# Kernel tuning notes

Measured on AMD Instinct MI355X. Metric: run time of the kernel, lower is better.

The kernel has to match this reference:

```python
import jax, jax.numpy as jnp
import numpy as np

EPS = 1e-8
BLOCK = 10  # proposals per frame; block-diagonal zeroing granularity


def _l2norm(x):
    # torch.norm(x, dim=-1, keepdim=True) + 1e-8
    return x / (jnp.linalg.norm(x, axis=-1, keepdims=True) + EPS)


def _block_mask(N):
    # For row j: zero cols [ (j//10)*10 , (j//10)*10 + 9 ) (i.e. 9 cols), then restore the diagonal.
    rows = jnp.arange(N)[:, None]
    cols = jnp.arange(N)[None, :]
    bstart = (rows // BLOCK) * BLOCK
    zeroed = (cols >= bstart) & (cols < bstart + (BLOCK - 1))
    keep = (~zeroed) | (rows == cols)
    return keep.astype(jnp.float32)  # [N, N]


def setup_inputs() -> dict:
    key = jax.random.key(0)
    k1, k2, k3, k4 = jax.random.split(key, 4)
    B, N, C = 1, 2000, 256
    x_cls = jax.random.normal(k1, (B, N, C), dtype=jnp.float32)
    x_reg = jax.random.normal(k2, (B, N, C), dtype=jnp.float32)
    s = 1.0 / np.sqrt(C)
    W_qkv_cls = jax.random.uniform(k3, (C, 3 * C), dtype=jnp.float32, minval=-s, maxval=s)
    W_qkv_reg = jax.random.uniform(k4, (C, 3 * C), dtype=jnp.float32, minval=-s, maxval=s)
    return {"x_cls": x_cls, "x_reg": x_reg, "W_qkv_cls": W_qkv_cls, "W_qkv_reg": W_qkv_reg}


def reference(x_cls, x_reg, W_qkv_cls, W_qkv_reg):
    num_heads = 8
    scale = 25.0
    sim_thresh = 0.75
    B, N, C = x_cls.shape
    hd = C // num_heads

    def qkv(x, W):
        # [B,N,3C] -> (3,B,H,N,hd)
        t = (x @ W).reshape(B, N, 3, num_heads, hd)
        return jnp.transpose(t, (2, 0, 3, 1, 4))

    q_cls, k_cls, v_cls = qkv(x_cls, W_qkv_cls)
    q_reg, k_reg, _v_reg = qkv(x_reg, W_qkv_reg)

    q_cls = _l2norm(q_cls)
    k_cls = _l2norm(k_cls)
    q_reg = _l2norm(q_reg)
    k_reg = _l2norm(k_reg)
    v_cls_normed = _l2norm(v_cls)

    # cosine-similarity of values (used for sim mask)
    attn_cls_raw = jnp.einsum('bhnd,bhmd->bhnm', v_cls_normed, v_cls_normed)

    attn_cls = jax.nn.softmax(jnp.einsum('bhnd,bhmd->bhnm', q_cls, k_cls) * scale, axis=-1)
    attn_reg = jax.nn.softmax(jnp.einsum('bhnd,bhmd->bhnm', q_reg, k_reg) * scale, axis=-1)
    attn = (attn_reg + attn_cls) * 0.5

    # block-diagonal zeroing (keeps diagonal), replacing the original CPU/numpy loop
    attn = attn * _block_mask(N)[None, None, :, :]

    x = jnp.einsum('bhnm,bhmd->bhnd', attn, v_cls)
    x = jnp.transpose(x, (0, 2, 1, 3)).reshape(B, N, C)
    x_ori = jnp.transpose(v_cls, (0, 2, 1, 3)).reshape(B, N, C)
    x_out = jnp.concatenate([x, x_ori], axis=-1)  # [B, N, 2C]

    # ave=True branch
    raw_mean = jnp.sum(attn_cls_raw, axis=1)[0] / num_heads          # [N, N]
    sim_mask = (raw_mean > sim_thresh).astype(jnp.float32)
    sim_attn = jnp.sum(attn, axis=1)[0] / num_heads                   # [N, N]
    sim_round2 = jax.nn.softmax(sim_attn, axis=-1)
    sim_round2 = sim_mask * sim_round2 / (jnp.sum(sim_mask * sim_round2, axis=-1, keepdims=True) + EPS)

    return (x_out, sim_round2)
```

## Files before the change

### kernel.cpp

```cpp
#include <hip/hip_runtime.h>
#include <math.h>

#define N_TOK 2000
#define NH 8
#define NHH 2
#define HD 32
#define SCALE 25.0f
#define SIM_TH 0.75f
#define EPSF 1e-8f
#define NT 125
#define QT 16

typedef _Float16 half2_t __attribute__((ext_vector_type(2)));
typedef _Float16 f16x4 __attribute__((ext_vector_type(4)));
typedef _Float16 f16x8 __attribute__((ext_vector_type(8)));
typedef float f32x4 __attribute__((ext_vector_type(4)));

__device__ __forceinline__ half2_t u2h(unsigned u) {
  return __builtin_bit_cast(half2_t, u);
}
__device__ __forceinline__ unsigned h2u(half2_t h) {
  return __builtin_bit_cast(unsigned, h);
}

__device__ __forceinline__ float fdot2f(unsigned a, unsigned b, float c) {
#if __has_builtin(__builtin_amdgcn_fdot2)
  return __builtin_amdgcn_fdot2(u2h(a), u2h(b), c, false);
#else
  const half2_t ha = u2h(a), hb = u2h(b);
  return c + (float)ha.x * (float)hb.x + (float)ha.y * (float)hb.y;
#endif
}

__device__ __forceinline__ float block_max256(float v, float* red) {
#pragma unroll
  for (int off = 32; off > 0; off >>= 1) v = fmaxf(v, __shfl_xor(v, off, 64));
  __syncthreads();
  if ((threadIdx.x & 63) == 0) red[threadIdx.x >> 6] = v;
  __syncthreads();
  return fmaxf(fmaxf(red[0], red[1]), fmaxf(red[2], red[3]));
}
__device__ __forceinline__ float block_sum256(float v, float* red) {
#pragma unroll
  for (int off = 32; off > 0; off >>= 1) v += __shfl_xor(v, off, 64);
  __syncthreads();
  if ((threadIdx.x & 63) == 0) red[threadIdx.x >> 6] = v;
  __syncthreads();
  return (red[0] + red[1]) + (red[2] + red[3]);
}

__global__ __launch_bounds__(256) void wpack_kernel(
    const float* __restrict__ W_cls, const float* __restrict__ W_reg,
    unsigned* __restrict__ Wp_cls, unsigned* __restrict__ Wp_reg) {
  const int idx = blockIdx.x * 256 + threadIdx.x;
  const int kq = idx / 768, c = idx % 768;
  const float* __restrict__ W = blockIdx.y ? W_reg : W_cls;
  uint4* __restrict__ Wq = (uint4*)(blockIdx.y ? Wp_reg : Wp_cls);
  uint4 o;
  o.x = h2u((half2_t){(_Float16)W[(8 * kq + 0) * 768 + c],
                      (_Float16)W[(8 * kq + 1) * 768 + c]});
  o.y = h2u((half2_t){(_Float16)W[(8 * kq + 2) * 768 + c],
                      (_Float16)W[(8 * kq + 3) * 768 + c]});
  o.z = h2u((half2_t){(_Float16)W[(8 * kq + 4) * 768 + c],
                      (_Float16)W[(8 * kq + 5) * 768 + c]});
  o.w = h2u((half2_t){(_Float16)W[(8 * kq + 6) * 768 + c],
                      (_Float16)W[(8 * kq + 7) * 768 + c]});
  Wq[idx] = o;
}

__global__ __launch_bounds__(256) void qkv_norm_kernel(
    const float* __restrict__ x_cls, const float* __restrict__ x_reg,
    const unsigned* __restrict__ Wp_cls, const unsigned* __restrict__ Wp_reg,
    _Float16* __restrict__ qc2, _Float16* __restrict__ qr2,
    _Float16* __restrict__ kc2, _Float16* __restrict__ kr2,
    _Float16* __restrict__ vn2, float* __restrict__ v_rm,
    _Float16* __restrict__ v_t) {
  __shared__ unsigned xs_p[8][128];
  __shared__ float res[8][768];
  __shared__ float inv_norm[192];

  const int n0 = blockIdx.x * 8;
  const int which = blockIdx.y;
  const int tid = threadIdx.x;
  const float* __restrict__ x = which ? x_reg : x_cls;
  const uint4* __restrict__ Wq = (const uint4*)(which ? Wp_reg : Wp_cls);

  if (tid < 128) {
#pragma unroll
    for (int r = 0; r < 8; r++) {
      const float2 xv = ((const float2*)x)[(size_t)(n0 + r) * 128 + tid];
      xs_p[r][tid] = h2u((half2_t){(_Float16)xv.x, (_Float16)xv.y});
    }
  }
  __syncthreads();

  float acc[8][3];
#pragma unroll
  for (int r = 0; r < 8; r++) acc[r][0] = acc[r][1] = acc[r][2] = 0.f;

  for (int kq = 0; kq < 32; kq++) {
    const uint4 w0 = Wq[kq * 768 + tid];
    const uint4 w1 = Wq[kq * 768 + tid + 256];
    const uint4 w2 = Wq[kq * 768 + tid + 512];
#pragma unroll
    for (int r = 0; r < 8; r++) {
      const uint4 xp = *(const uint4*)&xs_p[r][kq * 4];
      acc[r][0] = fdot2f(w0.x, xp.x, acc[r][0]);
      acc[r][0] = fdot2f(w0.y, xp.y, acc[r][0]);
      acc[r][0] = fdot2f(w0.z, xp.z, acc[r][0]);
      acc[r][0] = fdot2f(w0.w, xp.w, acc[r][0]);
      acc[r][1] = fdot2f(w1.x, xp.x, acc[r][1]);
      acc[r][1] = fdot2f(w1.y, xp.y, acc[r][1]);
      acc[r][1] = fdot2f(w1.z, xp.z, acc[r][1]);
      acc[r][1] = fdot2f(w1.w, xp.w, acc[r][1]);
      acc[r][2] = fdot2f(w2.x, xp.x, acc[r][2]);
      acc[r][2] = fdot2f(w2.y, xp.y, acc[r][2]);
      acc[r][2] = fdot2f(w2.z, xp.z, acc[r][2]);
      acc[r][2] = fdot2f(w2.w, xp.w, acc[r][2]);
    }
  }
#pragma unroll
  for (int r = 0; r < 8; r++) {
    res[r][tid] = acc[r][0];
    res[r][tid + 256] = acc[r][1];
    res[r][tid + 512] = acc[r][2];
  }
  __syncthreads();

  if (tid < 192) {
    const int r = tid / 24, grp = tid % 24;
    float ss = 0.f;
#pragma unroll
    for (int d = 0; d < HD; d++) {
      const float v = res[r][grp * 32 + d];
      ss += v * v;
    }
    inv_norm[tid] = 1.0f / (sqrtf(ss) + EPSF);
  }
  __syncthreads();

#pragma unroll
  for (int j = 0; j < 3; j++) {
    const int c = tid + j * 256;
    const int qkv = c >> 8, grp = c >> 5;
    const int h = grp & 7, d = c & 31;
#pragma unroll
    for (int r = 0; r < 8; r++) {
      const int n = n0 + r;
      const float val = res[r][c];
      const float nval = val * inv_norm[r * 24 + grp];
      const size_t fi = ((size_t)(h * N_TOK) + n) * HD + d;
      if (qkv == 0) {
        (which ? qr2 : qc2)[fi] = (_Float16)nval;
      } else if (qkv == 1) {
        (which ? kr2 : kc2)[fi] = (_Float16)nval;
      } else if (which == 0) {
        v_rm[fi] = val;
        vn2[fi] = (_Float16)nval;
        v_t[((size_t)(h * HD) + d) * N_TOK + n] = (_Float16)val;
      }
    }
  }
}

__global__ __launch_bounds__(256) void attn33_kernel(
    const _Float16* __restrict__ qc2, const _Float16* __restrict__ qr2,
    const _Float16* __restrict__ kc2, const _Float16* __restrict__ kr2,
    const _Float16* __restrict__ vn2, const _Float16* __restrict__ v_t,
    const float* __restrict__ v_rm, float* __restrict__ out_x,
    _Float16* __restrict__ sim_ws, _Float16* __restrict__ raw_ws) {
  __shared__ _Float16 qst[3][NHH][QT][40];
  __shared__ float smem_u[4224];

  float* __restrict__ sums_l = smem_u;
  float* __restrict__ nrm = smem_u + 256;
  float* __restrict__ st = smem_u;
  float* __restrict__ pvr = smem_u;

  const int tid = threadIdx.x;
  const int w = tid >> 6;
  const int l = tid & 63;
  const int qgrp = blockIdx.x >> 2;
  const int hp = blockIdx.x & 3;
  const int hq = hp * NHH;
  const int i0 = qgrp * QT;
  _Float16* __restrict__ simp = sim_ws + (size_t)hp * N_TOK * N_TOK;
  _Float16* __restrict__ rawp = raw_ws + (size_t)hp * N_TOK * N_TOK;

  if (tid < 128) {
    const int hh = tid >> 6, row = (tid >> 2) & 15, dg = tid & 3;
    const size_t src =
        ((size_t)((hq + hh) * N_TOK) + (i0 + row)) * HD + dg * 8;
    *(uint4*)&qst[0][hh][row][dg * 8] = *(const uint4*)(qc2 + src);
    *(uint4*)&qst[1][hh][row][dg * 8] = *(const uint4*)(qr2 + src);
    *(uint4*)&qst[2][hh][row][dg * 8] = *(const uint4*)(vn2 + src);
  }
  __syncthreads();

  const int q = l & 15;
  const int kg = l >> 4;
  const int i_glob = i0 + q;
  const int bs = (i_glob / 10) * 10;

  const f32x4 zero4 = {0.f, 0.f, 0.f, 0.f};

  float sc[NHH], sr[NHH];
#pragma unroll
  for (int hh = 0; hh < NHH; hh++) { sc[hh] = 0.f; sr[hh] = 0.f; }

  for (int t = w; t < NT; t += 4) {
    const int mb = t * 16;
#pragma unroll
    for (int hh = 0; hh < NHH; hh++) {
      const size_t koff =
          ((size_t)((hq + hh) * N_TOK) + mb + q) * HD + kg * 8;
      const f16x8 akc = *(const f16x8*)(kc2 + koff);
      const f16x8 akr = *(const f16x8*)(kr2 + koff);
      const f16x8 bqc = *(const f16x8*)&qst[0][hh][q][kg * 8];
      const f16x8 bqr = *(const f16x8*)&qst[1][hh][q][kg * 8];
      const f32x4 dc =
          __builtin_amdgcn_mfma_f32_16x16x32_f16(akc, bqc, zero4, 0, 0, 0);
      const f32x4 dr =
          __builtin_amdgcn_mfma_f32_16x16x32_f16(akr, bqr, zero4, 0, 0, 0);
#pragma unroll
      for (int i = 0; i < 4; i++) {
        sc[hh] += __expf(dc[i] * SCALE - SCALE);
        sr[hh] += __expf(dr[i] * SCALE - SCALE);
      }
    }
  }
#pragma unroll
  for (int hh = 0; hh < NHH; hh++) {
    sc[hh] += __shfl_xor(sc[hh], 16, 64);
    sc[hh] += __shfl_xor(sc[hh], 32, 64);
    sr[hh] += __shfl_xor(sr[hh], 16, 64);
    sr[hh] += __shfl_xor(sr[hh], 32, 64);
  }
  if (l < 16) {
#pragma unroll
    for (int hh = 0; hh < NHH; hh++) {
      sums_l[((w * 2 + 0) * NHH + hh) * 16 + l] = sc[hh];
      sums_l[((w * 2 + 1) * NHH + hh) * 16 + l] = sr[hh];
    }
  }
  __syncthreads();
  if (tid < 64) {
    const int pl = tid >> 5, hh = (tid >> 4) & 1, qq = tid & 15;
    const float s = sums_l[((0 * 2 + pl) * NHH + hh) * 16 + qq] +
                    sums_l[((1 * 2 + pl) * NHH + hh) * 16 + qq] +
                    sums_l[((2 * 2 + pl) * NHH + hh) * 16 + qq] +
                    sums_l[((3 * 2 + pl) * NHH + hh) * 16 + qq];
    nrm[(pl * NHH + hh) * 16 + qq] = 0.5f / s;
  }
  __syncthreads();
  float ncr[NHH], nrr[NHH];
#pragma unroll
  for (int hh = 0; hh < NHH; hh++) {
    ncr[hh] = nrm[(0 * NHH + hh) * 16 + q];
    nrr[hh] = nrm[(1 * NHH + hh) * 16 + q];
  }
  __syncthreads();

  f32x4 pv[NHH][2];
#pragma unroll
  for (int hh = 0; hh < NHH; hh++) { pv[hh][0] = zero4; pv[hh][1] = zero4; }

  for (int t = w; t < NT; t += 4) {
    const int mb = t * 16;
    f32x4 simt = zero4;
    f32x4 rawt = zero4;
#pragma unroll
    for (int hh = 0; hh < NHH; hh++) {
      const int h = hq + hh;
      const size_t koff = ((size_t)(h * N_TOK) + mb + q) * HD + kg * 8;
      const f16x8 akc = *(const f16x8*)(kc2 + koff);
      const f16x8 akr = *(const f16x8*)(kr2 + koff);
      const f16x8 avn = *(const f16x8*)(vn2 + koff);
      const f16x8 bqc = *(const f16x8*)&qst[0][hh][q][kg * 8];
      const f16x8 bqr = *(const f16x8*)&qst[1][hh][q][kg * 8];
      const f16x8 bqv = *(const f16x8*)&qst[2][hh][q][kg * 8];
      const f32x4 dc =
          __builtin_amdgcn_mfma_f32_16x16x32_f16(akc, bqc, zero4, 0, 0, 0);
      const f32x4 dr =
          __builtin_amdgcn_mfma_f32_16x16x32_f16(akr, bqr, zero4, 0, 0, 0);
      rawt = __builtin_amdgcn_mfma_f32_16x16x32_f16(avn, bqv, rawt, 0, 0, 0);

      f16x4 pa;
#pragma unroll
      for (int i = 0; i < 4; i++) {
        const float ec = __expf(dc[i] * SCALE - SCALE);
        const float er = __expf(dr[i] * SCALE - SCALE);
        float ai = ncr[hh] * ec + nrr[hh] * er;
        const int m = mb + kg * 4 + i;
        if (m >= bs && m < bs + 9 && m != i_glob) ai = 0.f;
        simt[i] += ai;
        pa[i] = (_Float16)ai;
      }
      const f16x4 bv0 = *(const f16x4*)(
          v_t + ((size_t)(h * HD) + q) * N_TOK + mb + kg * 4);
      const f16x4 bv1 = *(const f16x4*)(
          v_t + ((size_t)(h * HD) + 16 + q) * N_TOK + mb + kg * 4);
      pv[hh][0] =
          __builtin_amdgcn_mfma_f32_16x16x16f16(pa, bv0, pv[hh][0], 0, 0, 0);
      pv[hh][1] =
          __builtin_amdgcn_mfma_f32_16x16x16f16(pa, bv1, pv[hh][1], 0, 0, 0);
    }
    st[(w * 16 + q) * 20 + kg * 4 + 0] = simt[0];
    st[(w * 16 + q) * 20 + kg * 4 + 1] = simt[1];
    st[(w * 16 + q) * 20 + kg * 4 + 2] = simt[2];
    st[(w * 16 + q) * 20 + kg * 4 + 3] = simt[3];
    {
      const int row = l >> 2, mo = (l & 3) * 4;
      const float4 v4 = *(const float4*)&st[(w * 16 + row) * 20 + mo];
      uint2 u;
      u.x = h2u((half2_t){(_Float16)v4.x, (_Float16)v4.y});
      u.y = h2u((half2_t){(_Float16)v4.z, (_Float16)v4.w});
      *(uint2*)(simp + (size_t)(i0 + row) * N_TOK + mb + mo) = u;
    }
    st[(w * 16 + q) * 20 + kg * 4 + 0] = rawt[0];
    st[(w * 16 + q) * 20 + kg * 4 + 1] = rawt[1];
    st[(w * 16 + q) * 20 + kg * 4 + 2] = rawt[2];
    st[(w * 16 + q) * 20 + kg * 4 + 3] = rawt[3];
    {
      const int row = l >> 2, mo = (l & 3) * 4;
      const float4 v4 = *(const float4*)&st[(w * 16 + row) * 20 + mo];
      uint2 u;
      u.x = h2u((half2_t){(_Float16)v4.x, (_Float16)v4.y});
      u.y = h2u((half2_t){(_Float16)v4.z, (_Float16)v4.w});
      *(uint2*)(rawp + (size_t)(i0 + row) * N_TOK + mb + mo) = u;
    }
  }

  __syncthreads();
#pragma unroll
  for (int hh = 0; hh < NHH; hh++) {
#pragma unroll
    for (int i = 0; i < 4; i++) {
      pvr[((w * 2 + hh) * 16 + kg * 4 + i) * 33 + q] = pv[hh][0][i];
      pvr[((w * 2 + hh) * 16 + kg * 4 + i) * 33 + 16 + q] = pv[hh][1][i];
    }
  }
  __syncthreads();
  {
    const int hh = tid >> 7, qg2 = (tid >> 5) & 3, d = tid & 31;
#pragma unroll
    for (int qi = 0; qi < 4; qi++) {
      const int qq = qg2 * 4 + qi;
      float s = 0.f;
#pragma unroll
      for (int wv = 0; wv < 4; wv++) {
        s += pvr[((wv * 2 + hh) * 16 + qq) * 33 + d];
      }
      out_x[(size_t)(i0 + qq) * 512 + (hq + hh) * 32 + d] = s;
    }
  }
  if (tid < 64) {
    const int hh = tid >> 5, d = tid & 31;
    const int h = hq + hh;
#pragma unroll
    for (int qq = 0; qq < QT; qq++) {
      out_x[(size_t)(i0 + qq) * 512 + 256 + h * 32 + d] =
          v_rm[((size_t)(h * N_TOK) + i0 + qq) * HD + d];
    }
  }
}

__global__ __launch_bounds__(256) void sim_round2_kernel(
    const _Float16* __restrict__ sim_ws, const _Float16* __restrict__ raw_ws,
    float* __restrict__ out_sim) {
  __shared__ float red[16];
  const int tid = threadIdx.x;
  const int i0 = blockIdx.x * 8;
  const size_t NN = (size_t)N_TOK * N_TOK;
  for (int r = 0; r < 8; r++) {
    const int i = i0 + r;
    float s[8], rw[8];
#pragma unroll
    for (int t = 0; t < 8; t++) {
      const int m = tid + 256 * t;
      const bool valid = (t < 7) || (tid < 208);
      const size_t idx = (size_t)i * N_TOK + m;
      if (valid) {
        s[t] = ((float)sim_ws[idx] + (float)sim_ws[NN + idx] +
                (float)sim_ws[2 * NN + idx] + (float)sim_ws[3 * NN + idx]) *
               0.125f;
        rw[t] = (float)raw_ws[idx] + (float)raw_ws[NN + idx] +
                (float)raw_ws[2 * NN + idx] + (float)raw_ws[3 * NN + idx];
      } else {
        s[t] = -1e30f;
        rw[t] = 0.f;
      }
    }
    float lm = -1e30f;
#pragma unroll
    for (int t = 0; t < 8; t++) lm = fmaxf(lm, s[t]);
    const float M = block_max256(lm, red);
    float ls = 0.f;
#pragma unroll
    for (int t = 0; t < 8; t++) {
      const bool valid = (t < 7) || (tid < 208);
      const float e = valid ? __expf(s[t] - M) : 0.f;
      s[t] = e;
      ls += e;
    }
    const float S = block_sum256(ls, red);
    const float invS = 1.0f / S;
    float lms = 0.f;
#pragma unroll
    for (int t = 0; t < 8; t++) {
      const bool valid = (t < 7) || (tid < 208);
      const float p = s[t] * invS;
      const float mp = (valid && (rw[t] * 0.125f > SIM_TH)) ? p : 0.f;
      s[t] = mp;
      lms += mp;
    }
    const float MS = block_sum256(lms, red);
    const float invMS = 1.0f / (MS + EPSF);
#pragma unroll
    for (int t = 0; t < 8; t++) {
      const int m = tid + 256 * t;
      if ((t < 7) || (tid < 208)) {
        out_sim[(size_t)i * N_TOK + m] = s[t] * invMS;
      }
    }
  }
}

extern "C" void kernel_launch(void* const* d_in, const int* in_sizes, int n_in,
                              void* d_out, int out_size, void* d_ws,
                              size_t ws_size, hipStream_t stream) {
  const float* x_cls = (const float*)d_in[0];
  const float* x_reg = (const float*)d_in[1];
  const float* W_cls = (const float*)d_in[2];
  const float* W_reg = (const float*)d_in[3];

  const size_t seg = (size_t)NH * N_TOK * HD;
  float* v_rm = (float*)d_ws;
  _Float16* qc2 = (_Float16*)(v_rm + seg);
  _Float16* qr2 = qc2 + seg;
  _Float16* kc2 = qr2 + seg;
  _Float16* kr2 = kc2 + seg;
  _Float16* vn2 = kr2 + seg;
  _Float16* v_t = vn2 + seg;
  _Float16* sim_ws = v_t + seg;
  _Float16* raw_ws = sim_ws + 4 * (size_t)N_TOK * N_TOK;
  unsigned* Wp_cls = (unsigned*)(raw_ws + 4 * (size_t)N_TOK * N_TOK);
  unsigned* Wp_reg = Wp_cls + 98304;

  dim3 g0(96, 2);
  wpack_kernel<<<g0, 256, 0, stream>>>(W_cls, W_reg, Wp_cls, Wp_reg);

  dim3 g1(250, 2);
  qkv_norm_kernel<<<g1, 256, 0, stream>>>(x_cls, x_reg, Wp_cls, Wp_reg, qc2,
                                          qr2, kc2, kr2, vn2, v_rm, v_t);

  float* out_x = (float*)d_out;
  float* out_sim = out_x + (size_t)N_TOK * 512;
  attn33_kernel<<<500, 256, 0, stream>>>(qc2, qr2, kc2, kr2, vn2, v_t, v_rm,
                                         out_x, sim_ws, raw_ws);
  sim_round2_kernel<<<250, 256, 0, stream>>>(sim_ws, raw_ws, out_sim);
}
```

Baseline: 183.0 us.

## Compute QKV projection with MFMA using transposed fp16 weights

```diff
diff --git a/kernel.cpp b/kernel.cpp
--- a/kernel.cpp
+++ b/kernel.cpp
@@ -23,15 +23,6 @@
   return __builtin_bit_cast(unsigned, h);
 }
 
-__device__ __forceinline__ float fdot2f(unsigned a, unsigned b, float c) {
-#if __has_builtin(__builtin_amdgcn_fdot2)
-  return __builtin_amdgcn_fdot2(u2h(a), u2h(b), c, false);
-#else
-  const half2_t ha = u2h(a), hb = u2h(b);
-  return c + (float)ha.x * (float)hb.x + (float)ha.y * (float)hb.y;
-#endif
-}
-
 __device__ __forceinline__ float block_max256(float v, float* red) {
 #pragma unroll
   for (int off = 32; off > 0; off >>= 1) v = fmaxf(v, __shfl_xor(v, off, 64));
@@ -49,115 +40,114 @@
   return (red[0] + red[1]) + (red[2] + red[3]);
 }
 
-__global__ __launch_bounds__(256) void wpack_kernel(
+__global__ __launch_bounds__(256) void wpackT_kernel(
     const float* __restrict__ W_cls, const float* __restrict__ W_reg,
-    unsigned* __restrict__ Wp_cls, unsigned* __restrict__ Wp_reg) {
+    _Float16* __restrict__ Wt_cls, _Float16* __restrict__ Wt_reg) {
   const int idx = blockIdx.x * 256 + threadIdx.x;
-  const int kq = idx / 768, c = idx % 768;
+  const int kc = idx / 768;
+  const int n = idx % 768;
   const float* __restrict__ W = blockIdx.y ? W_reg : W_cls;
-  uint4* __restrict__ Wq = (uint4*)(blockIdx.y ? Wp_reg : Wp_cls);
+  _Float16* __restrict__ Wt = blockIdx.y ? Wt_reg : Wt_cls;
   uint4 o;
-  o.x = h2u((half2_t){(_Float16)W[(8 * kq + 0) * 768 + c],
-                      (_Float16)W[(8 * kq + 1) * 768 + c]});
-  o.y = h2u((half2_t){(_Float16)W[(8 * kq + 2) * 768 + c],
-                      (_Float16)W[(8 * kq + 3) * 768 + c]});
-  o.z = h2u((half2_t){(_Float16)W[(8 * kq + 4) * 768 + c],
-                      (_Float16)W[(8 * kq + 5) * 768 + c]});
-  o.w = h2u((half2_t){(_Float16)W[(8 * kq + 6) * 768 + c],
-                      (_Float16)W[(8 * kq + 7) * 768 + c]});
-  Wq[idx] = o;
-}
-
-__global__ __launch_bounds__(256) void qkv_norm_kernel(
+  o.x = h2u((half2_t){(_Float16)W[(kc * 8 + 0) * 768 + n],
+                      (_Float16)W[(kc * 8 + 1) * 768 + n]});
+  o.y = h2u((half2_t){(_Float16)W[(kc * 8 + 2) * 768 + n],
+                      (_Float16)W[(kc * 8 + 3) * 768 + n]});
+  o.z = h2u((half2_t){(_Float16)W[(kc * 8 + 4) * 768 + n],
+                      (_Float16)W[(kc * 8 + 5) * 768 + n]});
+  o.w = h2u((half2_t){(_Float16)W[(kc * 8 + 6) * 768 + n],
+                      (_Float16)W[(kc * 8 + 7) * 768 + n]});
+  *(uint4*)(Wt + (size_t)n * 256 + kc * 8) = o;
+}
+
+__global__ __launch_bounds__(256) void qkv_mfma_kernel(
     const float* __restrict__ x_cls, const float* __restrict__ x_reg,
-    const unsigned* __restrict__ Wp_cls, const unsigned* __restrict__ Wp_reg,
+    const _Float16* __restrict__ Wt_cls, const _Float16* __restrict__ Wt_reg,
     _Float16* __restrict__ qc2, _Float16* __restrict__ qr2,
     _Float16* __restrict__ kc2, _Float16* __restrict__ kr2,
     _Float16* __restrict__ vn2, float* __restrict__ v_rm,
     _Float16* __restrict__ v_t) {
-  __shared__ unsigned xs_p[8][128];
-  __shared__ float res[8][768];
-  __shared__ float inv_norm[192];
-
-  const int n0 = blockIdx.x * 8;
-  const int which = blockIdx.y;
+  __shared__ _Float16 xs[16][264];
+
   const int tid = threadIdx.x;
+  const int c = blockIdx.y;
+  const int which = (c >= 3) ? 1 : 0;
+  const int sec = which ? (c - 3) : c;
+  const int n0 = sec * 256;
+  const int i0 = blockIdx.x * 16;
   const float* __restrict__ x = which ? x_reg : x_cls;
-  const uint4* __restrict__ Wq = (const uint4*)(which ? Wp_reg : Wp_cls);
-
-  if (tid < 128) {
-#pragma unroll
-    for (int r = 0; r < 8; r++) {
-      const float2 xv = ((const float2*)x)[(size_t)(n0 + r) * 128 + tid];
-      xs_p[r][tid] = h2u((half2_t){(_Float16)xv.x, (_Float16)xv.y});
-    }
-  }
-  __syncthreads();
-
-  float acc[8][3];
-#pragma unroll
-  for (int r = 0; r < 8; r++) acc[r][0] = acc[r][1] = acc[r][2] = 0.f;
-
-  for (int kq = 0; kq < 32; kq++) {
-    const uint4 w0 = Wq[kq * 768 + tid];
-    const uint4 w1 = Wq[kq * 768 + tid + 256];
-    const uint4 w2 = Wq[kq * 768 + tid + 512];
-#pragma unroll
-    for (int r = 0; r < 8; r++) {
-      const uint4 xp = *(const uint4*)&xs_p[r][kq * 4];
-      acc[r][0] = fdot2f(w0.x, xp.x, acc[r][0]);
-      acc[r][0] = fdot2f(w0.y, xp.y, acc[r][0]);
-      acc[r][0] = fdot2f(w0.z, xp.z, acc[r][0]);
-      acc[r][0] = fdot2f(w0.w, xp.w, acc[r][0]);
-      acc[r][1] = fdot2f(w1.x, xp.x, acc[r][1]);
-      acc[r][1] = fdot2f(w1.y, xp.y, acc[r][1]);
-      acc[r][1] = fdot2f(w1.z, xp.z, acc[r][1]);
-      acc[r][1] = fdot2f(w1.w, xp.w, acc[r][1]);
-      acc[r][2] = fdot2f(w2.x, xp.x, acc[r][2]);
-      acc[r][2] = fdot2f(w2.y, xp.y, acc[r][2]);
-      acc[r][2] = fdot2f(w2.z, xp.z, acc[r][2]);
-      acc[r][2] = fdot2f(w2.w, xp.w, acc[r][2]);
-    }
-  }
-#pragma unroll
-  for (int r = 0; r < 8; r++) {
-    res[r][tid] = acc[r][0];
-    res[r][tid + 256] = acc[r][1];
-    res[r][tid + 512] = acc[r][2];
-  }
-  __syncthreads();
-
-  if (tid < 192) {
-    const int r = tid / 24, grp = tid % 24;
-    float ss = 0.f;
-#pragma unroll
-    for (int d = 0; d < HD; d++) {
-      const float v = res[r][grp * 32 + d];
-      ss += v * v;
-    }
-    inv_norm[tid] = 1.0f / (sqrtf(ss) + EPSF);
-  }
-  __syncthreads();
-
-#pragma unroll
-  for (int j = 0; j < 3; j++) {
-    const int c = tid + j * 256;
-    const int qkv = c >> 8, grp = c >> 5;
-    const int h = grp & 7, d = c & 31;
-#pragma unroll
-    for (int r = 0; r < 8; r++) {
-      const int n = n0 + r;
-      const float val = res[r][c];
-      const float nval = val * inv_norm[r * 24 + grp];
-      const size_t fi = ((size_t)(h * N_TOK) + n) * HD + d;
-      if (qkv == 0) {
-        (which ? qr2 : qc2)[fi] = (_Float16)nval;
-      } else if (qkv == 1) {
-        (which ? kr2 : kc2)[fi] = (_Float16)nval;
-      } else if (which == 0) {
-        v_rm[fi] = val;
-        vn2[fi] = (_Float16)nval;
-        v_t[((size_t)(h * HD) + d) * N_TOK + n] = (_Float16)val;
+  const _Float16* __restrict__ Wt = which ? Wt_reg : Wt_cls;
+
+  {
+    const int tok = tid >> 4, c4 = tid & 15;
+    const float4* __restrict__ xr =
+        (const float4*)(x + (size_t)(i0 + tok) * 256);
+#pragma unroll
+    for (int r = 0; r < 4; r++) {
+      const float4 v = xr[c4 + 16 * r];
+      *(unsigned*)&xs[tok][(c4 + 16 * r) * 4] =
+          h2u((half2_t){(_Float16)v.x, (_Float16)v.y});
+      *(unsigned*)&xs[tok][(c4 + 16 * r) * 4 + 2] =
+          h2u((half2_t){(_Float16)v.z, (_Float16)v.w});
+    }
+  }
+  __syncthreads();
+
+  const int w = tid >> 6, l = tid & 63;
+  const int q = l & 15, kg = l >> 4;
+  const f32x4 zero4 = {0.f, 0.f, 0.f, 0.f};
+  f32x4 acc[4] = {zero4, zero4, zero4, zero4};
+  const int nb = n0 + w * 64;
+
+#pragma unroll
+  for (int ks = 0; ks < 8; ks++) {
+    const int k0 = ks * 32;
+    const f16x8 bx = *(const f16x8*)&xs[q][k0 + kg * 8];
+#pragma unroll
+    for (int t2 = 0; t2 < 4; t2++) {
+      const f16x8 aw = *(const f16x8*)(
+          Wt + (size_t)(nb + t2 * 16 + q) * 256 + k0 + kg * 8);
+      acc[t2] =
+          __builtin_amdgcn_mfma_f32_16x16x32_f16(aw, bx, acc[t2], 0, 0, 0);
+    }
+  }
+
+  float ss0 = 0.f, ss1 = 0.f;
+#pragma unroll
+  for (int i = 0; i < 4; i++) {
+    ss0 += acc[0][i] * acc[0][i] + acc[1][i] * acc[1][i];
+    ss1 += acc[2][i] * acc[2][i] + acc[3][i] * acc[3][i];
+  }
+  ss0 += __shfl_xor(ss0, 16, 64);
+  ss0 += __shfl_xor(ss0, 32, 64);
+  ss1 += __shfl_xor(ss1, 16, 64);
+  ss1 += __shfl_xor(ss1, 32, 64);
+  const float inv0 = 1.0f / (sqrtf(ss0) + EPSF);
+  const float inv1 = 1.0f / (sqrtf(ss1) + EPSF);
+
+  const int tok = i0 + q;
+#pragma unroll
+  for (int t2 = 0; t2 < 4; t2++) {
+    const float inv = (t2 < 2) ? inv0 : inv1;
+    const int nrel = w * 64 + t2 * 16 + kg * 4;
+    const int h = nrel >> 5, d0 = nrel & 31;
+    uint2 un;
+    un.x = h2u((half2_t){(_Float16)(acc[t2][0] * inv),
+                         (_Float16)(acc[t2][1] * inv)});
+    un.y = h2u((half2_t){(_Float16)(acc[t2][2] * inv),
+                         (_Float16)(acc[t2][3] * inv)});
+    const size_t off = ((size_t)(h * N_TOK) + tok) * 32 + d0;
+    if (sec == 0) {
+      *(uint2*)((which ? qr2 : qc2) + off) = un;
+    } else if (sec == 1) {
+      *(uint2*)((which ? kr2 : kc2) + off) = un;
+    } else {
+      *(uint2*)(vn2 + off) = un;
+      const float4 vr = {acc[t2][0], acc[t2][1], acc[t2][2], acc[t2][3]};
+      *(float4*)(v_rm + off) = vr;
+#pragma unroll
+      for (int i = 0; i < 4; i++) {
+        v_t[((size_t)(h * 32) + d0 + i) * N_TOK + tok] = (_Float16)acc[t2][i];
       }
     }
   }
@@ -444,14 +434,14 @@
   _Float16* v_t = vn2 + seg;
   _Float16* sim_ws = v_t + seg;
   _Float16* raw_ws = sim_ws + 4 * (size_t)N_TOK * N_TOK;
-  unsigned* Wp_cls = (unsigned*)(raw_ws + 4 * (size_t)N_TOK * N_TOK);
-  unsigned* Wp_reg = Wp_cls + 98304;
+  _Float16* Wt_cls = raw_ws + 4 * (size_t)N_TOK * N_TOK;
+  _Float16* Wt_reg = Wt_cls + 768 * 256;
 
   dim3 g0(96, 2);
-  wpack_kernel<<<g0, 256, 0, stream>>>(W_cls, W_reg, Wp_cls, Wp_reg);
-
-  dim3 g1(250, 2);
-  qkv_norm_kernel<<<g1, 256, 0, stream>>>(x_cls, x_reg, Wp_cls, Wp_reg, qc2,
+  wpackT_kernel<<<g0, 256, 0, stream>>>(W_cls, W_reg, Wt_cls, Wt_reg);
+
+  dim3 g1(125, 5);
+  qkv_mfma_kernel<<<g1, 256, 0, stream>>>(x_cls, x_reg, Wt_cls, Wt_reg, qc2,
                                           qr2, kc2, kr2, vn2, v_rm, v_t);
 
   float* out_x = (float*)d_out;
```

Result: faster. 177.2 us (-3.1%).
